# Kernel tuning notes

Measured on AMD Instinct MI355X. Metric: run time of the kernel, lower is better.

Reference implementation:

```python
import jax, jax.numpy as jnp
import numpy as np

WINDOW = 7
N_HEADS = 4
EMBED = 128
N_TOK = WINDOW * WINDOW  # 49
N_WIN = 64               # windows per image (56x56 feature map / 7)
BATCH_IMG = 64
B = N_WIN * BATCH_IMG    # 4096


def make_rel_index(w):
    ch = np.arange(w)
    coords = np.stack(np.meshgrid(ch, ch), axis=0).reshape(2, -1)  # (2, w*w)
    rel = coords[:, :, None] - coords[:, None, :]                  # (2, N, N)
    rel = rel.transpose(1, 2, 0)
    rel[:, :, 0] += w - 1
    rel[:, :, 1] += w - 1
    rel[:, :, 0] *= 2 * w - 1
    return jnp.asarray(rel.sum(-1), dtype=jnp.int32)               # (N, N)


def setup_inputs() -> dict:
    key = jax.random.key(0)
    ks = jax.random.split(key, 6)
    x = jax.random.normal(ks[0], (B, N_TOK, EMBED), dtype=jnp.float32)
    qkv_w = jax.random.normal(ks[1], (EMBED, 3 * EMBED), dtype=jnp.float32) * (EMBED ** -0.5)
    qkv_b = jnp.zeros((3 * EMBED,), dtype=jnp.float32)
    proj_w = jax.random.normal(ks[2], (EMBED, EMBED), dtype=jnp.float32) * (EMBED ** -0.5)
    proj_b = jnp.zeros((EMBED,), dtype=jnp.float32)
    bias_table = jax.random.normal(ks[3], ((2 * WINDOW - 1) ** 2, N_HEADS), dtype=jnp.float32) * 0.02
    # shift mask: additive, 0 or large negative; use random binary * -100 to mimic Swin shift mask
    mask_bits = jax.random.bernoulli(ks[4], 0.2, (N_WIN, N_TOK, N_TOK))
    mask = jnp.where(mask_bits, jnp.float32(-100.0), jnp.float32(0.0))
    rel_index = make_rel_index(WINDOW)
    return {"x": x, "qkv_w": qkv_w, "qkv_b": qkv_b, "proj_w": proj_w,
            "proj_b": proj_b, "bias_table": bias_table, "mask": mask,
            "rel_index": rel_index}


def reference(x, qkv_w, qkv_b, proj_w, proj_b, bias_table, mask, rel_index):
    Bt, N, C = x.shape
    h = N_HEADS
    d = C // h
    scale = d ** -0.5
    qkv = (x @ qkv_w + qkv_b).reshape(Bt, N, 3, h, d)
    q, k, v = jnp.moveaxis(qkv, 2, 0)                      # each (B, N, h, d)
    q = q * scale
    attn = jnp.einsum('bnhd,bmhd->bhnm', q, k)             # (B, h, N, N)
    bias = bias_table[rel_index.reshape(-1)].reshape(N, N, h)
    attn = attn + jnp.transpose(bias, (2, 0, 1))[None]     # add rel-pos bias
    nW = mask.shape[0]
    attn = attn.reshape(Bt // nW, nW, h, N, N) + mask[None, :, None]
    attn = jax.nn.softmax(attn.reshape(Bt, h, N, N), axis=-1)
    out = jnp.einsum('bhnm,bmhd->bnhd', attn, v).reshape(Bt, N, C)
    return out @ proj_w + proj_b
```

## Files before the change

kernel.cpp:

```cpp
#include <hip/hip_runtime.h>

#define NTOK 49
#define CDIM 128
#define NH 4
#define NWIN 64

typedef unsigned short u16;
typedef unsigned int u32;
typedef __bf16 bf16x8 __attribute__((ext_vector_type(8)));
typedef float f32x4 __attribute__((ext_vector_type(4)));
typedef u16 u16x4 __attribute__((ext_vector_type(4)));

__device__ __forceinline__ u16 f2bf(float f) {
  u32 u = __float_as_uint(f);
  u += 0x7fffu + ((u >> 16) & 1u);
  return (u16)(u >> 16);
}
__device__ __forceinline__ u32 pack2(float a, float b) {
  return (u32)f2bf(a) | ((u32)f2bf(b) << 16);
}
__device__ __forceinline__ bf16x8 ld8(const u16* p) { return *(const bf16x8*)p; }

#define DPP_ADD(v, ctrl)                                                            \
  v += __int_as_float(__builtin_amdgcn_update_dpp(0, __float_as_int(v), ctrl, 0xf, 0xf, true))

__global__ void prep_kernel(const float* __restrict__ qkv_w,
                            const float* __restrict__ proj_w,
                            const float* __restrict__ bias_table,
                            const float* __restrict__ mask,
                            const int* __restrict__ rel_index,
                            u16* __restrict__ wqkvT,
                            u16* __restrict__ wprojT,
                            float* __restrict__ cmbT) {
  int i = blockIdx.x * 256 + threadIdx.x;
  if (i < 384 * 128) {
    int n = i >> 7, k = i & 127;
    wqkvT[i] = f2bf(qkv_w[k * 384 + n]);
  }
  if (i < 128 * 128) {
    int n = i >> 7, k = i & 127;
    wprojT[i] = f2bf(proj_w[k * 128 + n]);
  }
  int n = i & 63, m = (i >> 6) & 63, hh = (i >> 12) & 3, win = i >> 14;
  float v = -1e30f;
  if (n < NTOK && m < NTOK)
    v = bias_table[rel_index[n * NTOK + m] * NH + hh] + mask[(win * NTOK + n) * NTOK + m];
  cmbT[i] = v;
}

#define RGN(h) (8192 + (h) * 4608)

__device__ __forceinline__ int xsw(int row, int col) {
  return (row << 7) + ((((col >> 3) ^ (row & 15)) << 3) | (col & 7));
}

__global__ __launch_bounds__(256, 3)
void swin_fused(const float* __restrict__ x, const float* __restrict__ qkv_b,
                const float* __restrict__ proj_b, const u16* __restrict__ wqkvT,
                const u16* __restrict__ wprojT, const float* __restrict__ cmbT,
                float* __restrict__ out) {
  __shared__ u16 lds[26624];
  const int tid  = threadIdx.x;
  const int w    = tid >> 6;
  const int lane = tid & 63;
  const int ln   = lane & 15;
  const int quad = lane >> 4;
  const int b    = blockIdx.x;
  const int win  = b & (NWIN - 1);
  const float scale = 0.17677669529663687f;

  {
    const float4* x4 = (const float4*)(x + (size_t)b * (NTOK * CDIM));
    for (int i = tid; i < (NTOK * CDIM) / 4; i += 256) {
      float4 f = x4[i];
      int e = i << 2;
      int row = e >> 7, col = e & 127;
      u16x4 v;
      v[0] = f2bf(f.x); v[1] = f2bf(f.y); v[2] = f2bf(f.z); v[3] = f2bf(f.w);
      *(u16x4*)&lds[xsw(row, col)] = v;
    }
    for (int i = tid; i < (15 * CDIM) / 4; i += 256) {
      int e = i << 2;
      int row = NTOK + (e >> 7), col = e & 127;
      u16x4 v = {0, 0, 0, 0};
      *(u16x4*)&lds[xsw(row, col)] = v;
    }
  }
  __syncthreads();

  u32 vbx[4][2], vby[4][2];
  {
    bf16x8 af[4][4];
#pragma unroll
    for (int tm = 0; tm < 4; ++tm)
#pragma unroll
      for (int ks = 0; ks < 4; ++ks)
        af[tm][ks] = ld8(&lds[xsw(tm * 16 + ln, ks * 32 + quad * 8)]);

#pragma unroll
    for (int tl = 0; tl < 6; ++tl) {
      int sect = tl >> 1, tc = tl & 1;
      int colg = sect * 128 + w * 32 + tc * 16 + ln;
      bf16x8 bw[4];
#pragma unroll
      for (int ks = 0; ks < 4; ++ks)
        bw[ks] = ld8(wqkvT + colg * 128 + ks * 32 + quad * 8);
      float cb = qkv_b[colg];
#pragma unroll
      for (int tm = 0; tm < 4; ++tm) {
        f32x4 acc = {0.f, 0.f, 0.f, 0.f};
#pragma unroll
        for (int ks = 0; ks < 4; ++ks)
          acc = __builtin_amdgcn_mfma_f32_16x16x32_bf16(af[tm][ks], bw[ks], acc, 0, 0, 0);
        int row0 = tm * 16 + quad * 4;
        if (sect == 0) {
#pragma unroll
          for (int r = 0; r < 4; ++r)
            lds[RGN(w) + (row0 + r) * 36 + tc * 16 + ln] = f2bf((acc[r] + cb) * scale);
        } else if (sect == 1) {
#pragma unroll
          for (int r = 0; r < 4; ++r)
            lds[RGN(w) + 2304 + (row0 + r) * 36 + tc * 16 + ln] = f2bf(acc[r] + cb);
        } else {
          vbx[tm][tc] = pack2(acc[0] + cb, acc[1] + cb);
          vby[tm][tc] = pack2(acc[2] + cb, acc[3] + cb);
        }
      }
    }
  }

  f32x4 s[4][4];
  {
    bf16x8 aq[4];
#pragma unroll
    for (int tm = 0; tm < 4; ++tm)
      aq[tm] = ld8(&lds[RGN(w) + (tm * 16 + ln) * 36 + quad * 8]);
#pragma unroll
    for (int tn = 0; tn < 4; ++tn) {
      bf16x8 bk = ld8(&lds[RGN(w) + 2304 + (tn * 16 + ln) * 36 + quad * 8]);
#pragma unroll
      for (int tm = 0; tm < 4; ++tm) {
        f32x4 z = {0.f, 0.f, 0.f, 0.f};
        s[tm][tn] = __builtin_amdgcn_mfma_f32_16x16x32_bf16(aq[tm], bk, z, 0, 0, 0);
      }
    }
  }
  {
    const float* cb = cmbT + ((size_t)((win << 2) | w) << 12);
#pragma unroll
    for (int tm = 0; tm < 4; ++tm) {
#pragma unroll
      for (int tn = 0; tn < 4; ++tn) {
        f32x4 c4 = *(const f32x4*)&cb[(tn * 16 + ln) * 64 + tm * 16 + quad * 4];
        s[tm][tn] += c4;
      }
    }
  }
  float inv[4][4];
#pragma unroll
  for (int tm = 0; tm < 4; ++tm) {
    int row0 = tm * 16 + quad * 4;
#pragma unroll
    for (int r = 0; r < 4; ++r) {
      float e0 = __expf(s[tm][0][r]);
      float e1 = __expf(s[tm][1][r]);
      float e2 = __expf(s[tm][2][r]);
      float e3 = __expf(s[tm][3][r]);
      float t = (e0 + e1) + (e2 + e3);
      DPP_ADD(t, 0xB1);
      DPP_ADD(t, 0x4E);
      DPP_ADD(t, 0x124);
      DPP_ADD(t, 0x128);
      inv[tm][r] = 1.0f / t;
      int rr = row0 + r;
      lds[RGN(w) + rr * 68 + 0 * 16 + ln] = f2bf(e0);
      lds[RGN(w) + rr * 68 + 1 * 16 + ln] = f2bf(e1);
      lds[RGN(w) + rr * 68 + 2 * 16 + ln] = f2bf(e2);
      lds[RGN(w) + rr * 68 + 3 * 16 + ln] = f2bf(e3);
    }
  }

  {
    f32x4 o[4][2];
#pragma unroll
    for (int tm = 0; tm < 4; ++tm)
#pragma unroll
      for (int tc = 0; tc < 2; ++tc) { f32x4 z = {0.f,0.f,0.f,0.f}; o[tm][tc] = z; }
#pragma unroll
    for (int ks = 0; ks < 2; ++ks) {
      bf16x8 pa[4];
#pragma unroll
      for (int tm = 0; tm < 4; ++tm)
        pa[tm] = ld8(&lds[RGN(w) + (tm * 16 + ln) * 68 + ks * 32 + quad * 8]);
#pragma unroll
      for (int tc = 0; tc < 2; ++tc) {
        union { u32 u[4]; bf16x8 v; } bv;
#pragma unroll
        for (int p = 0; p < 4; ++p) {
          int src = ((2 * (quad & 1) + (p >> 1)) << 4) | ln;
          int a0 = __shfl((int)((p & 1) ? vby[2 * ks][tc]     : vbx[2 * ks][tc]),     src);
          int a1 = __shfl((int)((p & 1) ? vby[2 * ks + 1][tc] : vbx[2 * ks + 1][tc]), src);
          bv.u[p] = (u32)((quad < 2) ? a0 : a1);
        }
#pragma unroll
        for (int tm = 0; tm < 4; ++tm)
          o[tm][tc] = __builtin_amdgcn_mfma_f32_16x16x32_bf16(pa[tm], bv.v, o[tm][tc], 0, 0, 0);
      }
    }
#pragma unroll
    for (int tm = 0; tm < 4; ++tm) {
      int row0 = tm * 16 + quad * 4;
#pragma unroll
      for (int tc = 0; tc < 2; ++tc)
#pragma unroll
        for (int r = 0; r < 4; ++r)
          lds[RGN(w) + 2304 + (row0 + r) * 36 + tc * 16 + ln] = f2bf(o[tm][tc][r] * inv[tm][r]);
    }
  }
  __syncthreads();

  {
    bf16x8 aof[4][4];
#pragma unroll
    for (int tm = 0; tm < 4; ++tm)
#pragma unroll
      for (int ks = 0; ks < 4; ++ks)
        aof[tm][ks] = ld8(&lds[RGN(ks) + 2304 + (tm * 16 + ln) * 36 + quad * 8]);
#pragma unroll
    for (int tj = 0; tj < 2; ++tj) {
      int colg = w * 32 + tj * 16 + ln;
      bf16x8 bw[4];
#pragma unroll
      for (int ks = 0; ks < 4; ++ks)
        bw[ks] = ld8(wprojT + colg * 128 + ks * 32 + quad * 8);
      float pb = proj_b[colg];
#pragma unroll
      for (int tm = 0; tm < 4; ++tm) {
        f32x4 acc = {0.f, 0.f, 0.f, 0.f};
#pragma unroll
        for (int ks = 0; ks < 4; ++ks)
          acc = __builtin_amdgcn_mfma_f32_16x16x32_bf16(aof[tm][ks], bw[ks], acc, 0, 0, 0);
        int row0 = tm * 16 + quad * 4;
#pragma unroll
        for (int r = 0; r < 4; ++r) {
          int rr = row0 + r;
          if (rr < NTOK)
            out[((size_t)b * NTOK + rr) * CDIM + colg] = acc[r] + pb;
        }
      }
    }
  }
}

extern "C" void kernel_launch(void* const* d_in, const int* in_sizes, int n_in,
                              void* d_out, int out_size, void* d_ws, size_t ws_size,
                              hipStream_t stream) {
  const float* x          = (const float*)d_in[0];
  const float* qkv_w      = (const float*)d_in[1];
  const float* qkv_b      = (const float*)d_in[2];
  const float* proj_w     = (const float*)d_in[3];
  const float* proj_b     = (const float*)d_in[4];
  const float* bias_table = (const float*)d_in[5];
  const float* mask       = (const float*)d_in[6];
  const int*   rel_index  = (const int*)d_in[7];

  u16*   wqkvT  = (u16*)d_ws;
  u16*   wprojT = wqkvT + 384 * 128;
  float* cmbT   = (float*)((char*)d_ws + 131072);

  const int Bt = in_sizes[0] / (NTOK * CDIM);

  prep_kernel<<<4096, 256, 0, stream>>>(qkv_w, proj_w, bias_table, mask, rel_index,
                                        wqkvT, wprojT, cmbT);
  swin_fused<<<Bt, 256, 0, stream>>>(x, qkv_b, proj_b, wqkvT, wprojT, cmbT, (float*)d_out);
}
```

Measured before the change: 303.3 us.

## Load x fragments directly from global into registers, shrink LDS, raise occupancy

Removes the LDS staging of the x tile: each lane now reads its MFMA A-fragments straight from global memory as float4 pairs and converts them to bf16 in registers. This drops the swizzled LDS writes, a barrier and the LDS reads, and frees 8192 u16 of shared memory, so the LDS regions shift down and launch bounds go from 3 to 4 blocks per CU. The bf16 conversion switches to the native __bf16 cast. In exchange each x element is fetched by its own lanes with strided global loads instead of coalesced bulk loads, and register pressure under the tighter occupancy bound may cause spills.

Measured after the change: 314.4 us. +3.7%, slower.

```diff
diff --git a/kernel.cpp b/kernel.cpp
--- a/kernel.cpp
+++ b/kernel.cpp
@@ -12,9 +12,9 @@
 typedef u16 u16x4 __attribute__((ext_vector_type(4)));
 
 __device__ __forceinline__ u16 f2bf(float f) {
-  u32 u = __float_as_uint(f);
-  u += 0x7fffu + ((u >> 16) & 1u);
-  return (u16)(u >> 16);
+  union { __bf16 h; u16 u; } c;
+  c.h = (__bf16)f;
+  return c.u;
 }
 __device__ __forceinline__ u32 pack2(float a, float b) {
   return (u32)f2bf(a) | ((u32)f2bf(b) << 16);
@@ -48,18 +48,14 @@
   cmbT[i] = v;
 }
 
-#define RGN(h) (8192 + (h) * 4608)
-
-__device__ __forceinline__ int xsw(int row, int col) {
-  return (row << 7) + ((((col >> 3) ^ (row & 15)) << 3) | (col & 7));
-}
-
-__global__ __launch_bounds__(256, 3)
+#define RGN(h) ((h) * 4608)
+
+__global__ __launch_bounds__(256, 4)
 void swin_fused(const float* __restrict__ x, const float* __restrict__ qkv_b,
                 const float* __restrict__ proj_b, const u16* __restrict__ wqkvT,
                 const u16* __restrict__ wprojT, const float* __restrict__ cmbT,
                 float* __restrict__ out) {
-  __shared__ u16 lds[26624];
+  __shared__ u16 lds[18432];
   const int tid  = threadIdx.x;
   const int w    = tid >> 6;
   const int lane = tid & 63;
@@ -69,33 +65,25 @@
   const int win  = b & (NWIN - 1);
   const float scale = 0.17677669529663687f;
 
-  {
-    const float4* x4 = (const float4*)(x + (size_t)b * (NTOK * CDIM));
-    for (int i = tid; i < (NTOK * CDIM) / 4; i += 256) {
-      float4 f = x4[i];
-      int e = i << 2;
-      int row = e >> 7, col = e & 127;
-      u16x4 v;
-      v[0] = f2bf(f.x); v[1] = f2bf(f.y); v[2] = f2bf(f.z); v[3] = f2bf(f.w);
-      *(u16x4*)&lds[xsw(row, col)] = v;
-    }
-    for (int i = tid; i < (15 * CDIM) / 4; i += 256) {
-      int e = i << 2;
-      int row = NTOK + (e >> 7), col = e & 127;
-      u16x4 v = {0, 0, 0, 0};
-      *(u16x4*)&lds[xsw(row, col)] = v;
-    }
-  }
-  __syncthreads();
-
   u32 vbx[4][2], vby[4][2];
   {
     bf16x8 af[4][4];
-#pragma unroll
-    for (int tm = 0; tm < 4; ++tm)
-#pragma unroll
-      for (int ks = 0; ks < 4; ++ks)
-        af[tm][ks] = ld8(&lds[xsw(tm * 16 + ln, ks * 32 + quad * 8)]);
+    const float* xb = x + (size_t)b * (NTOK * CDIM);
+#pragma unroll
+    for (int tm = 0; tm < 4; ++tm) {
+      int row = tm * 16 + ln;
+      const float4* rp = (const float4*)(xb + row * CDIM) + (quad << 1);
+      bool ok = (tm < 3) | (row < NTOK);
+#pragma unroll
+      for (int ks = 0; ks < 4; ++ks) {
+        float4 f0 = {0.f, 0.f, 0.f, 0.f}, f1 = {0.f, 0.f, 0.f, 0.f};
+        if (ok) { f0 = rp[ks * 8]; f1 = rp[ks * 8 + 1]; }
+        bf16x8 v;
+        v[0] = (__bf16)f0.x; v[1] = (__bf16)f0.y; v[2] = (__bf16)f0.z; v[3] = (__bf16)f0.w;
+        v[4] = (__bf16)f1.x; v[5] = (__bf16)f1.y; v[6] = (__bf16)f1.z; v[7] = (__bf16)f1.w;
+        af[tm][ks] = v;
+      }
+    }
 
 #pragma unroll
     for (int tl = 0; tl < 6; ++tl) {
```

## Split each head across two waves with 512-thread blocks

Applied to the files above, without the earlier changes.

Doubles the block to 8 waves so each head's query rows are split between two waves, with each wave computing half the Q/K rows while both compute the full V tile. Extra barriers are added because Q/K and the probability matrix are now shared across waves through LDS. The bf16 conversion also switches to the native cast. The aim is shorter per-wave dependency chains and lower register pressure, in exchange for redundant V projection work, more synchronisation and heavier LDS use per CU.

After: 418.8 us. +38.1%, slower.

```diff
diff --git a/kernel.cpp b/kernel.cpp
--- a/kernel.cpp
+++ b/kernel.cpp
@@ -12,9 +12,9 @@
 typedef u16 u16x4 __attribute__((ext_vector_type(4)));
 
 __device__ __forceinline__ u16 f2bf(float f) {
-  u32 u = __float_as_uint(f);
-  u += 0x7fffu + ((u >> 16) & 1u);
-  return (u16)(u >> 16);
+  union { __bf16 h; u16 u; } c;
+  c.h = (__bf16)f;
+  return c.u;
 }
 __device__ __forceinline__ u32 pack2(float a, float b) {
   return (u32)f2bf(a) | ((u32)f2bf(b) << 16);
@@ -54,14 +54,16 @@
   return (row << 7) + ((((col >> 3) ^ (row & 15)) << 3) | (col & 7));
 }
 
-__global__ __launch_bounds__(256, 3)
+__global__ __launch_bounds__(512, 6)
 void swin_fused(const float* __restrict__ x, const float* __restrict__ qkv_b,
                 const float* __restrict__ proj_b, const u16* __restrict__ wqkvT,
                 const u16* __restrict__ wprojT, const float* __restrict__ cmbT,
                 float* __restrict__ out) {
   __shared__ u16 lds[26624];
   const int tid  = threadIdx.x;
-  const int w    = tid >> 6;
+  const int wave = tid >> 6;
+  const int head = wave & 3;
+  const int hh   = wave >> 2;
   const int lane = tid & 63;
   const int ln   = lane & 15;
   const int quad = lane >> 4;
@@ -71,7 +73,7 @@
 
   {
     const float4* x4 = (const float4*)(x + (size_t)b * (NTOK * CDIM));
-    for (int i = tid; i < (NTOK * CDIM) / 4; i += 256) {
+    for (int i = tid; i < (NTOK * CDIM) / 4; i += 512) {
       float4 f = x4[i];
       int e = i << 2;
       int row = e >> 7, col = e & 127;
@@ -79,7 +81,7 @@
       v[0] = f2bf(f.x); v[1] = f2bf(f.y); v[2] = f2bf(f.z); v[3] = f2bf(f.w);
       *(u16x4*)&lds[xsw(row, col)] = v;
     }
-    for (int i = tid; i < (15 * CDIM) / 4; i += 256) {
+    for (int i = tid; i < (15 * CDIM) / 4; i += 512) {
       int e = i << 2;
       int row = NTOK + (e >> 7), col = e & 127;
       u16x4 v = {0, 0, 0, 0};
@@ -90,17 +92,46 @@
 
   u32 vbx[4][2], vby[4][2];
   {
-    bf16x8 af[4][4];
-#pragma unroll
-    for (int tm = 0; tm < 4; ++tm)
+    bf16x8 afh[2][4];
+#pragma unroll
+    for (int t = 0; t < 2; ++t)
 #pragma unroll
       for (int ks = 0; ks < 4; ++ks)
-        af[tm][ks] = ld8(&lds[xsw(tm * 16 + ln, ks * 32 + quad * 8)]);
-
-#pragma unroll
-    for (int tl = 0; tl < 6; ++tl) {
-      int sect = tl >> 1, tc = tl & 1;
-      int colg = sect * 128 + w * 32 + tc * 16 + ln;
+        afh[t][ks] = ld8(&lds[xsw((2 * hh + t) * 16 + ln, ks * 32 + quad * 8)]);
+
+#pragma unroll
+    for (int sect = 0; sect < 2; ++sect) {
+#pragma unroll
+      for (int tc = 0; tc < 2; ++tc) {
+        int colg = sect * 128 + head * 32 + tc * 16 + ln;
+        bf16x8 bw[4];
+#pragma unroll
+        for (int ks = 0; ks < 4; ++ks)
+          bw[ks] = ld8(wqkvT + colg * 128 + ks * 32 + quad * 8);
+        float cb = qkv_b[colg];
+#pragma unroll
+        for (int t = 0; t < 2; ++t) {
+          f32x4 acc = {0.f, 0.f, 0.f, 0.f};
+#pragma unroll
+          for (int ks = 0; ks < 4; ++ks)
+            acc = __builtin_amdgcn_mfma_f32_16x16x32_bf16(afh[t][ks], bw[ks], acc, 0, 0, 0);
+          int row0 = (2 * hh + t) * 16 + quad * 4;
+          if (sect == 0) {
+#pragma unroll
+            for (int r = 0; r < 4; ++r)
+              lds[RGN(head) + (row0 + r) * 36 + tc * 16 + ln] = f2bf((acc[r] + cb) * scale);
+          } else {
+#pragma unroll
+            for (int r = 0; r < 4; ++r)
+              lds[RGN(head) + 2304 + (row0 + r) * 36 + tc * 16 + ln] = f2bf(acc[r] + cb);
+          }
+        }
+      }
+    }
+
+#pragma unroll
+    for (int tc = 0; tc < 2; ++tc) {
+      int colg = 256 + head * 32 + tc * 16 + ln;
       bf16x8 bw[4];
 #pragma unroll
       for (int ks = 0; ks < 4; ++ks)
@@ -108,90 +139,95 @@
       float cb = qkv_b[colg];
 #pragma unroll
       for (int tm = 0; tm < 4; ++tm) {
+        bf16x8 afv[4];
+#pragma unroll
+        for (int ks = 0; ks < 4; ++ks)
+          afv[ks] = ld8(&lds[xsw(tm * 16 + ln, ks * 32 + quad * 8)]);
         f32x4 acc = {0.f, 0.f, 0.f, 0.f};
 #pragma unroll
         for (int ks = 0; ks < 4; ++ks)
-          acc = __builtin_amdgcn_mfma_f32_16x16x32_bf16(af[tm][ks], bw[ks], acc, 0, 0, 0);
-        int row0 = tm * 16 + quad * 4;
-        if (sect == 0) {
-#pragma unroll
-          for (int r = 0; r < 4; ++r)
-            lds[RGN(w) + (row0 + r) * 36 + tc * 16 + ln] = f2bf((acc[r] + cb) * scale);
-        } else if (sect == 1) {
-#pragma unroll
-          for (int r = 0; r < 4; ++r)
-            lds[RGN(w) + 2304 + (row0 + r) * 36 + tc * 16 + ln] = f2bf(acc[r] + cb);
-        } else {
-          vbx[tm][tc] = pack2(acc[0] + cb, acc[1] + cb);
-          vby[tm][tc] = pack2(acc[2] + cb, acc[3] + cb);
-        }
-      }
-    }
-  }
-
-  f32x4 s[4][4];
-  {
-    bf16x8 aq[4];
-#pragma unroll
-    for (int tm = 0; tm < 4; ++tm)
-      aq[tm] = ld8(&lds[RGN(w) + (tm * 16 + ln) * 36 + quad * 8]);
+          acc = __builtin_amdgcn_mfma_f32_16x16x32_bf16(afv[ks], bw[ks], acc, 0, 0, 0);
+        vbx[tm][tc] = pack2(acc[0] + cb, acc[1] + cb);
+        vby[tm][tc] = pack2(acc[2] + cb, acc[3] + cb);
+      }
+    }
+  }
+  __syncthreads();
+
+  f32x4 s[2][4];
+  {
+    bf16x8 aq[2];
+#pragma unroll
+    for (int t = 0; t < 2; ++t)
+      aq[t] = ld8(&lds[RGN(head) + ((2 * hh + t) * 16 + ln) * 36 + quad * 8]);
 #pragma unroll
     for (int tn = 0; tn < 4; ++tn) {
-      bf16x8 bk = ld8(&lds[RGN(w) + 2304 + (tn * 16 + ln) * 36 + quad * 8]);
-#pragma unroll
-      for (int tm = 0; tm < 4; ++tm) {
+      bf16x8 bk = ld8(&lds[RGN(head) + 2304 + (tn * 16 + ln) * 36 + quad * 8]);
+#pragma unroll
+      for (int t = 0; t < 2; ++t) {
         f32x4 z = {0.f, 0.f, 0.f, 0.f};
-        s[tm][tn] = __builtin_amdgcn_mfma_f32_16x16x32_bf16(aq[tm], bk, z, 0, 0, 0);
-      }
-    }
-  }
-  {
-    const float* cb = cmbT + ((size_t)((win << 2) | w) << 12);
-#pragma unroll
-    for (int tm = 0; tm < 4; ++tm) {
+        s[t][tn] = __builtin_amdgcn_mfma_f32_16x16x32_bf16(aq[t], bk, z, 0, 0, 0);
+      }
+    }
+  }
+  {
+    const float* cb = cmbT + ((size_t)((win << 2) | head) << 12);
+#pragma unroll
+    for (int t = 0; t < 2; ++t) {
 #pragma unroll
       for (int tn = 0; tn < 4; ++tn) {
-        f32x4 c4 = *(const f32x4*)&cb[(tn * 16 + ln) * 64 + tm * 16 + quad * 4];
-        s[tm][tn] += c4;
-      }
-    }
-  }
-  float inv[4][4];
-#pragma unroll
-  for (int tm = 0; tm < 4; ++tm) {
-    int row0 = tm * 16 + quad * 4;
+        f32x4 c4 = *(const f32x4*)&cb[(tn * 16 + ln) * 64 + (2 * hh + t) * 16 + quad * 4];
+        s[t][tn] += c4;
+      }
+    }
+  }
+  float inv[2][4];
+  float ev[2][4][4];
+#pragma unroll
+  for (int t = 0; t < 2; ++t) {
 #pragma unroll
     for (int r = 0; r < 4; ++r) {
-      float e0 = __expf(s[tm][0][r]);
-      float e1 = __expf(s[tm][1][r]);
-      float e2 = __expf(s[tm][2][r]);
-      float e3 = __expf(s[tm][3][r]);
-      float t = (e0 + e1) + (e2 + e3);
-      DPP_ADD(t, 0xB1);
-      DPP_ADD(t, 0x4E);
-      DPP_ADD(t, 0x124);
-      DPP_ADD(t, 0x128);
-      inv[tm][r] = 1.0f / t;
-      int rr = row0 + r;
-      lds[RGN(w) + rr * 68 + 0 * 16 + ln] = f2bf(e0);
-      lds[RGN(w) + rr * 68 + 1 * 16 + ln] = f2bf(e1);
-      lds[RGN(w) + rr * 68 + 2 * 16 + ln] = f2bf(e2);
-      lds[RGN(w) + rr * 68 + 3 * 16 + ln] = f2bf(e3);
-    }
-  }
-
-  {
-    f32x4 o[4][2];
-#pragma unroll
-    for (int tm = 0; tm < 4; ++tm)
-#pragma unroll
-      for (int tc = 0; tc < 2; ++tc) { f32x4 z = {0.f,0.f,0.f,0.f}; o[tm][tc] = z; }
+      float e0 = __expf(s[t][0][r]);
+      float e1 = __expf(s[t][1][r]);
+      float e2 = __expf(s[t][2][r]);
+      float e3 = __expf(s[t][3][r]);
+      float tt = (e0 + e1) + (e2 + e3);
+      DPP_ADD(tt, 0xB1);
+      DPP_ADD(tt, 0x4E);
+      DPP_ADD(tt, 0x124);
+      DPP_ADD(tt, 0x128);
+      inv[t][r] = 1.0f / tt;
+      ev[t][0][r] = e0; ev[t][1][r] = e1; ev[t][2][r] = e2; ev[t][3][r] = e3;
+    }
+  }
+  __syncthreads();
+#pragma unroll
+  for (int t = 0; t < 2; ++t) {
+#pragma unroll
+    for (int r = 0; r < 4; ++r) {
+      int rr = (2 * hh + t) * 16 + quad * 4 + r;
+      lds[RGN(head) + rr * 68 + 0 * 16 + ln] = f2bf(ev[t][0][r]);
+      lds[RGN(head) + rr * 68 + 1 * 16 + ln] = f2bf(ev[t][1][r]);
+      lds[RGN(head) + rr * 68 + 2 * 16 + ln] = f2bf(ev[t][2][r]);
+      lds[RGN(head) + rr * 68 + 3 * 16 + ln] = f2bf(ev[t][3][r]);
+    }
+  }
+
+  {
+    bf16x8 pa[2][2];
+#pragma unroll
+    for (int t = 0; t < 2; ++t)
+#pragma unroll
+      for (int ks = 0; ks < 2; ++ks)
+        pa[t][ks] = ld8(&lds[RGN(head) + ((2 * hh + t) * 16 + ln) * 68 + ks * 32 + quad * 8]);
+    __syncthreads();
+    f32x4 o[2][2];
+#pragma unroll
+    for (int t = 0; t < 2; ++t)
+#pragma unroll
+      for (int tc = 0; tc < 2; ++tc) { f32x4 z = {0.f,0.f,0.f,0.f}; o[t][tc] = z; }
 #pragma unroll
     for (int ks = 0; ks < 2; ++ks) {
-      bf16x8 pa[4];
-#pragma unroll
-      for (int tm = 0; tm < 4; ++tm)
-        pa[tm] = ld8(&lds[RGN(w) + (tm * 16 + ln) * 68 + ks * 32 + quad * 8]);
 #pragma unroll
       for (int tc = 0; tc < 2; ++tc) {
         union { u32 u[4]; bf16x8 v; } bv;
@@ -203,44 +239,44 @@
           bv.u[p] = (u32)((quad < 2) ? a0 : a1);
         }
 #pragma unroll
-        for (int tm = 0; tm < 4; ++tm)
-          o[tm][tc] = __builtin_amdgcn_mfma_f32_16x16x32_bf16(pa[tm], bv.v, o[tm][tc], 0, 0, 0);
-      }
-    }
-#pragma unroll
-    for (int tm = 0; tm < 4; ++tm) {
-      int row0 = tm * 16 + quad * 4;
+        for (int t = 0; t < 2; ++t)
+          o[t][tc] = __builtin_amdgcn_mfma_f32_16x16x32_bf16(pa[t][ks], bv.v, o[t][tc], 0, 0, 0);
+      }
+    }
+#pragma unroll
+    for (int t = 0; t < 2; ++t) {
+      int row0 = (2 * hh + t) * 16 + quad * 4;
 #pragma unroll
       for (int tc = 0; tc < 2; ++tc)
 #pragma unroll
         for (int r = 0; r < 4; ++r)
-          lds[RGN(w) + 2304 + (row0 + r) * 36 + tc * 16 + ln] = f2bf(o[tm][tc][r] * inv[tm][r]);
+          lds[RGN(head) + 2304 + (row0 + r) * 36 + tc * 16 + ln] = f2bf(o[t][tc][r] * inv[t][r]);
     }
   }
   __syncthreads();
 
   {
-    bf16x8 aof[4][4];
-#pragma unroll
-    for (int tm = 0; tm < 4; ++tm)
+    bf16x8 aof[2][4];
+#pragma unroll
+    for (int t = 0; t < 2; ++t)
 #pragma unroll
       for (int ks = 0; ks < 4; ++ks)
-        aof[tm][ks] = ld8(&lds[RGN(ks) + 2304 + (tm * 16 + ln) * 36 + quad * 8]);
+        aof[t][ks] = ld8(&lds[RGN(ks) + 2304 + ((2 * hh + t) * 16 + ln) * 36 + quad * 8]);
 #pragma unroll
     for (int tj = 0; tj < 2; ++tj) {
-      int colg = w * 32 + tj * 16 + ln;
+      int colg = head * 32 + tj * 16 + ln;
       bf16x8 bw[4];
 #pragma unroll
       for (int ks = 0; ks < 4; ++ks)
         bw[ks] = ld8(wprojT + colg * 128 + ks * 32 + quad * 8);
       float pb = proj_b[colg];
 #pragma unroll
-      for (int tm = 0; tm < 4; ++tm) {
+      for (int t = 0; t < 2; ++t) {
         f32x4 acc = {0.f, 0.f, 0.f, 0.f};
 #pragma unroll
         for (int ks = 0; ks < 4; ++ks)
-          acc = __builtin_amdgcn_mfma_f32_16x16x32_bf16(aof[tm][ks], bw[ks], acc, 0, 0, 0);
-        int row0 = tm * 16 + quad * 4;
+          acc = __builtin_amdgcn_mfma_f32_16x16x32_bf16(aof[t][ks], bw[ks], acc, 0, 0, 0);
+        int row0 = (2 * hh + t) * 16 + quad * 4;
 #pragma unroll
         for (int r = 0; r < 4; ++r) {
           int rr = row0 + r;
@@ -272,5 +308,5 @@
 
   prep_kernel<<<4096, 256, 0, stream>>>(qkv_w, proj_w, bias_table, mask, rel_index,
                                         wqkvT, wprojT, cmbT);
-  swin_fused<<<Bt, 256, 0, stream>>>(x, qkv_b, proj_b, wqkvT, wprojT, cmbT, (float*)d_out);
-}
+  swin_fused<<<Bt, 512, 0, stream>>>(x, qkv_b, proj_b, wqkvT, wprojT, cmbT, (float*)d_out);
+}
```

## Keep Q/K/P in registers via transposed MFMA, fuse softmax into PV loop

Applied to the files above, without the earlier changes.

Q and K are computed as transposed MFMA outputs and kept packed in registers. Operand fragments are then built with lane shuffles instead of being staged through per-head LDS regions. Scores are exponentiated and fed straight into the PV MFMAs in half-row chunks, with row sums reduced by shuffles. This shrinks LDS from about 52KB to 34KB, and launch bounds are raised from 3 to 4 blocks per CU. The risks are higher register pressure and extra cross-lane shuffle traffic, and bf16 conversion now uses the native cast.

Measured after the change: 427.2 us. 1.41x slower.

```diff
diff --git a/kernel.cpp b/kernel.cpp
--- a/kernel.cpp
+++ b/kernel.cpp
@@ -11,18 +11,28 @@
 typedef float f32x4 __attribute__((ext_vector_type(4)));
 typedef u16 u16x4 __attribute__((ext_vector_type(4)));
 
+union Frag { u32 u[4]; bf16x8 v; };
+
 __device__ __forceinline__ u16 f2bf(float f) {
-  u32 u = __float_as_uint(f);
-  u += 0x7fffu + ((u >> 16) & 1u);
-  return (u16)(u >> 16);
+  union { __bf16 h; u16 u; } c;
+  c.h = (__bf16)f;
+  return c.u;
 }
 __device__ __forceinline__ u32 pack2(float a, float b) {
   return (u32)f2bf(a) | ((u32)f2bf(b) << 16);
 }
 __device__ __forceinline__ bf16x8 ld8(const u16* p) { return *(const bf16x8*)p; }
 
-#define DPP_ADD(v, ctrl)                                                            \
-  v += __int_as_float(__builtin_amdgcn_update_dpp(0, __float_as_int(v), ctrl, 0xf, 0xf, true))
+__device__ __forceinline__ void build_frag(u32 u[4], u32 x0, u32 y0, u32 x1, u32 y1,
+                                           int quad, int ln) {
+#pragma unroll
+  for (int p = 0; p < 4; ++p) {
+    int src = ((2 * (quad & 1) + (p >> 1)) << 4) | ln;
+    int a0 = __shfl((int)((p & 1) ? y0 : x0), src);
+    int a1 = __shfl((int)((p & 1) ? y1 : x1), src);
+    u[p] = (u32)((quad < 2) ? a0 : a1);
+  }
+}
 
 __global__ void prep_kernel(const float* __restrict__ qkv_w,
                             const float* __restrict__ proj_w,
@@ -31,7 +41,7 @@
                             const int* __restrict__ rel_index,
                             u16* __restrict__ wqkvT,
                             u16* __restrict__ wprojT,
-                            float* __restrict__ cmbT) {
+                            float* __restrict__ cmb) {
   int i = blockIdx.x * 256 + threadIdx.x;
   if (i < 384 * 128) {
     int n = i >> 7, k = i & 127;
@@ -41,27 +51,27 @@
     int n = i >> 7, k = i & 127;
     wprojT[i] = f2bf(proj_w[k * 128 + n]);
   }
-  int n = i & 63, m = (i >> 6) & 63, hh = (i >> 12) & 3, win = i >> 14;
+  int m = i & 63, q = (i >> 6) & 63, hh = (i >> 12) & 3, win = i >> 14;
   float v = -1e30f;
-  if (n < NTOK && m < NTOK)
-    v = bias_table[rel_index[n * NTOK + m] * NH + hh] + mask[(win * NTOK + n) * NTOK + m];
-  cmbT[i] = v;
-}
-
-#define RGN(h) (8192 + (h) * 4608)
+  if (q < NTOK && m < NTOK)
+    v = bias_table[rel_index[q * NTOK + m] * NH + hh] + mask[(win * NTOK + q) * NTOK + m];
+  cmb[i] = v;
+}
+
+#define AOFF 8192
 
 __device__ __forceinline__ int xsw(int row, int col) {
   return (row << 7) + ((((col >> 3) ^ (row & 15)) << 3) | (col & 7));
 }
 
-__global__ __launch_bounds__(256, 3)
+__global__ __launch_bounds__(256, 4)
 void swin_fused(const float* __restrict__ x, const float* __restrict__ qkv_b,
                 const float* __restrict__ proj_b, const u16* __restrict__ wqkvT,
-                const u16* __restrict__ wprojT, const float* __restrict__ cmbT,
+                const u16* __restrict__ wprojT, const float* __restrict__ cmb,
                 float* __restrict__ out) {
-  __shared__ u16 lds[26624];
+  __shared__ u16 lds[17408];
   const int tid  = threadIdx.x;
-  const int w    = tid >> 6;
+  const int head = tid >> 6;
   const int lane = tid & 63;
   const int ln   = lane & 15;
   const int quad = lane >> 4;
@@ -88,133 +98,123 @@
   }
   __syncthreads();
 
-  u32 vbx[4][2], vby[4][2];
+  u32 qx[4][2], qy[4][2], kx[4][2], ky[4][2], vbx[4][2], vby[4][2];
   {
-    bf16x8 af[4][4];
-#pragma unroll
-    for (int tm = 0; tm < 4; ++tm)
+#pragma unroll
+    for (int tm = 0; tm < 4; ++tm) {
+      bf16x8 af[4];
 #pragma unroll
       for (int ks = 0; ks < 4; ++ks)
-        af[tm][ks] = ld8(&lds[xsw(tm * 16 + ln, ks * 32 + quad * 8)]);
-
-#pragma unroll
-    for (int tl = 0; tl < 6; ++tl) {
-      int sect = tl >> 1, tc = tl & 1;
-      int colg = sect * 128 + w * 32 + tc * 16 + ln;
-      bf16x8 bw[4];
-#pragma unroll
-      for (int ks = 0; ks < 4; ++ks)
-        bw[ks] = ld8(wqkvT + colg * 128 + ks * 32 + quad * 8);
-      float cb = qkv_b[colg];
-#pragma unroll
-      for (int tm = 0; tm < 4; ++tm) {
+        af[ks] = ld8(&lds[xsw(tm * 16 + ln, ks * 32 + quad * 8)]);
+#pragma unroll
+      for (int sect = 0; sect < 2; ++sect) {
+#pragma unroll
+        for (int tc = 0; tc < 2; ++tc) {
+          int colb = sect * 128 + head * 32 + tc * 16;
+          bf16x8 bw[4];
+#pragma unroll
+          for (int ks = 0; ks < 4; ++ks)
+            bw[ks] = ld8(wqkvT + (colb + ln) * 128 + ks * 32 + quad * 8);
+          f32x4 cb4 = *(const f32x4*)&qkv_b[colb + quad * 4];
+          f32x4 acc = {0.f, 0.f, 0.f, 0.f};
+#pragma unroll
+          for (int ks = 0; ks < 4; ++ks)
+            acc = __builtin_amdgcn_mfma_f32_16x16x32_bf16(bw[ks], af[ks], acc, 0, 0, 0);
+          if (sect == 0) {
+            qx[tm][tc] = pack2((acc[0] + cb4[0]) * scale, (acc[1] + cb4[1]) * scale);
+            qy[tm][tc] = pack2((acc[2] + cb4[2]) * scale, (acc[3] + cb4[3]) * scale);
+          } else {
+            kx[tm][tc] = pack2(acc[0] + cb4[0], acc[1] + cb4[1]);
+            ky[tm][tc] = pack2(acc[2] + cb4[2], acc[3] + cb4[3]);
+          }
+        }
+      }
+#pragma unroll
+      for (int tc = 0; tc < 2; ++tc) {
+        int colg = 256 + head * 32 + tc * 16 + ln;
+        bf16x8 bw[4];
+#pragma unroll
+        for (int ks = 0; ks < 4; ++ks)
+          bw[ks] = ld8(wqkvT + colg * 128 + ks * 32 + quad * 8);
+        float cb = qkv_b[colg];
         f32x4 acc = {0.f, 0.f, 0.f, 0.f};
 #pragma unroll
         for (int ks = 0; ks < 4; ++ks)
-          acc = __builtin_amdgcn_mfma_f32_16x16x32_bf16(af[tm][ks], bw[ks], acc, 0, 0, 0);
-        int row0 = tm * 16 + quad * 4;
-        if (sect == 0) {
-#pragma unroll
-          for (int r = 0; r < 4; ++r)
-            lds[RGN(w) + (row0 + r) * 36 + tc * 16 + ln] = f2bf((acc[r] + cb) * scale);
-        } else if (sect == 1) {
-#pragma unroll
-          for (int r = 0; r < 4; ++r)
-            lds[RGN(w) + 2304 + (row0 + r) * 36 + tc * 16 + ln] = f2bf(acc[r] + cb);
-        } else {
-          vbx[tm][tc] = pack2(acc[0] + cb, acc[1] + cb);
-          vby[tm][tc] = pack2(acc[2] + cb, acc[3] + cb);
+          acc = __builtin_amdgcn_mfma_f32_16x16x32_bf16(af[ks], bw[ks], acc, 0, 0, 0);
+        vbx[tm][tc] = pack2(acc[0] + cb, acc[1] + cb);
+        vby[tm][tc] = pack2(acc[2] + cb, acc[3] + cb);
+      }
+    }
+  }
+
+#pragma unroll
+  for (int tmh = 0; tmh < 2; ++tmh) {
+    Frag qf[2];
+#pragma unroll
+    for (int t2 = 0; t2 < 2; ++t2) {
+      int tm = 2 * tmh + t2;
+      build_frag(qf[t2].u, qx[tm][0], qy[tm][0], qx[tm][1], qy[tm][1], quad, ln);
+    }
+    f32x4 o[2][2];
+#pragma unroll
+    for (int t2 = 0; t2 < 2; ++t2)
+#pragma unroll
+      for (int tc = 0; tc < 2; ++tc) { f32x4 z = {0.f,0.f,0.f,0.f}; o[t2][tc] = z; }
+    float rs[2] = {0.f, 0.f};
+
+#pragma unroll
+    for (int tnp = 0; tnp < 2; ++tnp) {
+      u32 px[2][2], py[2][2];
+#pragma unroll
+      for (int tn2 = 0; tn2 < 2; ++tn2) {
+        int tn = 2 * tnp + tn2;
+        Frag kf;
+        build_frag(kf.u, kx[tn][0], ky[tn][0], kx[tn][1], ky[tn][1], quad, ln);
+#pragma unroll
+        for (int t2 = 0; t2 < 2; ++t2) {
+          f32x4 z = {0.f, 0.f, 0.f, 0.f};
+          f32x4 s4 = __builtin_amdgcn_mfma_f32_16x16x32_bf16(kf.v, qf[t2].v, z, 0, 0, 0);
+          const float* cp = cmb + (((size_t)((win << 2) | head)) << 12)
+                          + ((2 * tmh + t2) * 16 + ln) * 64 + tn * 16 + quad * 4;
+          f32x4 c4 = *(const f32x4*)cp;
+          float e0 = __expf(s4[0] + c4[0]);
+          float e1 = __expf(s4[1] + c4[1]);
+          float e2 = __expf(s4[2] + c4[2]);
+          float e3 = __expf(s4[3] + c4[3]);
+          rs[t2] += (e0 + e1) + (e2 + e3);
+          px[tn2][t2] = pack2(e0, e1);
+          py[tn2][t2] = pack2(e2, e3);
         }
       }
-    }
-  }
-
-  f32x4 s[4][4];
-  {
-    bf16x8 aq[4];
-#pragma unroll
-    for (int tm = 0; tm < 4; ++tm)
-      aq[tm] = ld8(&lds[RGN(w) + (tm * 16 + ln) * 36 + quad * 8]);
-#pragma unroll
-    for (int tn = 0; tn < 4; ++tn) {
-      bf16x8 bk = ld8(&lds[RGN(w) + 2304 + (tn * 16 + ln) * 36 + quad * 8]);
-#pragma unroll
-      for (int tm = 0; tm < 4; ++tm) {
-        f32x4 z = {0.f, 0.f, 0.f, 0.f};
-        s[tm][tn] = __builtin_amdgcn_mfma_f32_16x16x32_bf16(aq[tm], bk, z, 0, 0, 0);
-      }
-    }
-  }
-  {
-    const float* cb = cmbT + ((size_t)((win << 2) | w) << 12);
-#pragma unroll
-    for (int tm = 0; tm < 4; ++tm) {
-#pragma unroll
-      for (int tn = 0; tn < 4; ++tn) {
-        f32x4 c4 = *(const f32x4*)&cb[(tn * 16 + ln) * 64 + tm * 16 + quad * 4];
-        s[tm][tn] += c4;
-      }
-    }
-  }
-  float inv[4][4];
-#pragma unroll
-  for (int tm = 0; tm < 4; ++tm) {
-    int row0 = tm * 16 + quad * 4;
-#pragma unroll
-    for (int r = 0; r < 4; ++r) {
-      float e0 = __expf(s[tm][0][r]);
-      float e1 = __expf(s[tm][1][r]);
-      float e2 = __expf(s[tm][2][r]);
-      float e3 = __expf(s[tm][3][r]);
-      float t = (e0 + e1) + (e2 + e3);
-      DPP_ADD(t, 0xB1);
-      DPP_ADD(t, 0x4E);
-      DPP_ADD(t, 0x124);
-      DPP_ADD(t, 0x128);
-      inv[tm][r] = 1.0f / t;
-      int rr = row0 + r;
-      lds[RGN(w) + rr * 68 + 0 * 16 + ln] = f2bf(e0);
-      lds[RGN(w) + rr * 68 + 1 * 16 + ln] = f2bf(e1);
-      lds[RGN(w) + rr * 68 + 2 * 16 + ln] = f2bf(e2);
-      lds[RGN(w) + rr * 68 + 3 * 16 + ln] = f2bf(e3);
-    }
-  }
-
-  {
-    f32x4 o[4][2];
-#pragma unroll
-    for (int tm = 0; tm < 4; ++tm)
-#pragma unroll
-      for (int tc = 0; tc < 2; ++tc) { f32x4 z = {0.f,0.f,0.f,0.f}; o[tm][tc] = z; }
-#pragma unroll
-    for (int ks = 0; ks < 2; ++ks) {
-      bf16x8 pa[4];
-#pragma unroll
-      for (int tm = 0; tm < 4; ++tm)
-        pa[tm] = ld8(&lds[RGN(w) + (tm * 16 + ln) * 68 + ks * 32 + quad * 8]);
+      Frag pa[2];
+#pragma unroll
+      for (int t2 = 0; t2 < 2; ++t2)
+        build_frag(pa[t2].u, px[0][t2], py[0][t2], px[1][t2], py[1][t2], quad, ln);
 #pragma unroll
       for (int tc = 0; tc < 2; ++tc) {
-        union { u32 u[4]; bf16x8 v; } bv;
-#pragma unroll
-        for (int p = 0; p < 4; ++p) {
-          int src = ((2 * (quad & 1) + (p >> 1)) << 4) | ln;
-          int a0 = __shfl((int)((p & 1) ? vby[2 * ks][tc]     : vbx[2 * ks][tc]),     src);
-          int a1 = __shfl((int)((p & 1) ? vby[2 * ks + 1][tc] : vbx[2 * ks + 1][tc]), src);
-          bv.u[p] = (u32)((quad < 2) ? a0 : a1);
-        }
-#pragma unroll
-        for (int tm = 0; tm < 4; ++tm)
-          o[tm][tc] = __builtin_amdgcn_mfma_f32_16x16x32_bf16(pa[tm], bv.v, o[tm][tc], 0, 0, 0);
-      }
-    }
-#pragma unroll
-    for (int tm = 0; tm < 4; ++tm) {
-      int row0 = tm * 16 + quad * 4;
-#pragma unroll
-      for (int tc = 0; tc < 2; ++tc)
-#pragma unroll
-        for (int r = 0; r < 4; ++r)
-          lds[RGN(w) + 2304 + (row0 + r) * 36 + tc * 16 + ln] = f2bf(o[tm][tc][r] * inv[tm][r]);
+        Frag bv;
+        build_frag(bv.u, vbx[2 * tnp][tc], vby[2 * tnp][tc],
+                   vbx[2 * tnp + 1][tc], vby[2 * tnp + 1][tc], quad, ln);
+#pragma unroll
+        for (int t2 = 0; t2 < 2; ++t2)
+          o[t2][tc] = __builtin_amdgcn_mfma_f32_16x16x32_bf16(pa[t2].v, bv.v, o[t2][tc], 0, 0, 0);
+      }
+    }
+
+#pragma unroll
+    for (int t2 = 0; t2 < 2; ++t2) {
+      float t = rs[t2];
+      t += __shfl_xor(t, 16);
+      t += __shfl_xor(t, 32);
+      float iv = 1.0f / fmaxf(t, 1e-30f);
+#pragma unroll
+      for (int r = 0; r < 4; ++r) {
+        float ivr = __shfl(iv, quad * 4 + r);
+        int row = (2 * tmh + t2) * 16 + quad * 4 + r;
+#pragma unroll
+        for (int tc = 0; tc < 2; ++tc)
+          lds[AOFF + head * 2304 + row * 36 + tc * 16 + ln] = f2bf(o[t2][tc][r] * ivr);
+      }
     }
   }
   __syncthreads();
@@ -225,10 +225,10 @@
     for (int tm = 0; tm < 4; ++tm)
 #pragma unroll
       for (int ks = 0; ks < 4; ++ks)
-        aof[tm][ks] = ld8(&lds[RGN(ks) + 2304 + (tm * 16 + ln) * 36 + quad * 8]);
+        aof[tm][ks] = ld8(&lds[AOFF + ks * 2304 + (tm * 16 + ln) * 36 + quad * 8]);
 #pragma unroll
     for (int tj = 0; tj < 2; ++tj) {
-      int colg = w * 32 + tj * 16 + ln;
+      int colg = head * 32 + tj * 16 + ln;
       bf16x8 bw[4];
 #pragma unroll
       for (int ks = 0; ks < 4; ++ks)
@@ -266,11 +266,11 @@
 
   u16*   wqkvT  = (u16*)d_ws;
   u16*   wprojT = wqkvT + 384 * 128;
-  float* cmbT   = (float*)((char*)d_ws + 131072);
+  float* cmb    = (float*)((char*)d_ws + 131072);
 
   const int Bt = in_sizes[0] / (NTOK * CDIM);
 
   prep_kernel<<<4096, 256, 0, stream>>>(qkv_w, proj_w, bias_table, mask, rel_index,
-                                        wqkvT, wprojT, cmbT);
-  swin_fused<<<Bt, 256, 0, stream>>>(x, qkv_b, proj_b, wqkvT, wprojT, cmbT, (float*)d_out);
-}
+                                        wqkvT, wprojT, cmb);
+  swin_fused<<<Bt, 256, 0, stream>>>(x, qkv_b, proj_b, wqkvT, wprojT, cmb, (float*)d_out);
+}
```
